# Performance work log

Measured on AMD Instinct MI355X. Metric: run time of the kernel, lower is better.

The kernel has to match this reference:

```python
import jax, jax.numpy as jnp
import numpy as np

CODE_DIMS = [32, 32, 16]   # prod = 16384 out features
FEAT_DIM = 1024
EPS = 1e-6


def setup_inputs() -> dict:
    key = jax.random.key(0)
    kx, kw = jax.random.split(key)
    x = jax.random.normal(kx, (4, 2048, FEAT_DIM), dtype=jnp.float32)
    # per-chunk trunc-normal init like _init_weights: std = sqrt(2/(feat_dim+code_dim)), clipped at +-3 std
    parts = []
    for i, cd in enumerate(CODE_DIMS):
        std = float(np.sqrt(2.0 / (FEAT_DIM + cd)))
        parts.append(std * jax.random.truncated_normal(
            jax.random.fold_in(kw, i), -3.0, 3.0, (cd, FEAT_DIM), dtype=jnp.float32))
    weight = jnp.concatenate(parts, axis=0)  # (sum(code_dims)=80, feat_dim)
    return {"x": x, "weight": weight}


def _rms_norm(y):
    var = jnp.mean(y * y, axis=-1, keepdims=True) + EPS
    return y * jax.lax.rsqrt(var)


def reference(x, weight):
    # split weight rows into the low-rank factors
    a, b, c = jnpp_split = jnp.split(weight, np.cumsum(CODE_DIMS)[:-1].tolist(), axis=0)
    # outer product over code dims, shared feature axis z -> dynamic weight (prod(code_dims), feat_dim)
    W = jnp.einsum('az,bz,cz->abcz', a, b, c).reshape(-1, weight.shape[-1])
    y = jnp.einsum('bsi,oi->bso', x, W)  # dense projection
    return _rms_norm(y)
```

## Files before the change

kernel.cpp:

```cpp
#include <hip/hip_runtime.h>
#include <hip/hip_bf16.h>

typedef unsigned short u16;
typedef __attribute__((ext_vector_type(8))) short bf16x8;
typedef __attribute__((ext_vector_type(4))) float f32x4;
typedef __attribute__((ext_vector_type(8))) unsigned short ushort8;

#define FEAT 1024
#define NOUT 16384
#define EPS 1e-6f
#define NT 16

#define GLOBAL_AS __attribute__((address_space(1)))
#define LDS_AS __attribute__((address_space(3)))

__device__ __forceinline__ void load16_to_lds(const u16* g, u16* l) {
    __builtin_amdgcn_global_load_lds((const GLOBAL_AS void*)g, (LDS_AS void*)l, 16, 0, 0);
}

__device__ __forceinline__ u16 f32_to_bf16_bits(float f) {
    __hip_bfloat16 h = __float2bfloat16(f);
    return *reinterpret_cast<u16*>(&h);
}

__device__ __forceinline__ float bf16_bits_to_f32(u16 b) {
    unsigned u = ((unsigned)b) << 16;
    float f;
    __builtin_memcpy(&f, &u, 4);
    return f;
}

__global__ void wbuild_kernel(const float* __restrict__ w, u16* __restrict__ Wb) {
    const int t  = blockIdx.x * 256 + threadIdx.x;
    const int o  = t >> 7;
    const int k0 = (t & 127) << 3;
    const int ai = o >> 9;
    const int bi = (o >> 4) & 31;
    const int ci = o & 15;
    const float* A = w + ai * FEAT + k0;
    const float* B = w + (32 + bi) * FEAT + k0;
    const float* C = w + (64 + ci) * FEAT + k0;
    ushort8 r;
#pragma unroll
    for (int j = 0; j < 8; ++j) r[j] = f32_to_bf16_bits(A[j] * B[j] * C[j]);
    *reinterpret_cast<ushort8*>(Wb + (size_t)t * 8) = r;
}

__global__ void xcast_kernel(const float* __restrict__ x, u16* __restrict__ Xb) {
    const int t = blockIdx.x * 256 + threadIdx.x;
    const float4* xv = reinterpret_cast<const float4*>(x) + (size_t)t * 2;
    const float4 f0 = xv[0];
    const float4 f1 = xv[1];
    float vals[8] = {f0.x, f0.y, f0.z, f0.w, f1.x, f1.y, f1.z, f1.w};
    ushort8 r;
#pragma unroll
    for (int j = 0; j < 8; ++j) r[j] = f32_to_bf16_bits(vals[j]);
    *reinterpret_cast<ushort8*>(Xb + (size_t)t * 8) = r;
}


#define LDSOFF(buf, isB, kh) (((buf) << 15) + ((isB) << 14) + ((kh) << 13))

#define STAGE(isB, tt, kh, buf) do {                                          \
    const u16* g = ((isB) ? gB : gA) + (size_t)(tt) * 64 + (kh) * 32 + w * 32768; \
    u16* l = lds + LDSOFF(buf, isB, kh) + w * 1024;                           \
    load16_to_lds(g, l);                                                      \
    load16_to_lds(g + 16384, l + 512);                                        \
} while (0)

#define RD_A(dst, mi, ks, buf) dst = *reinterpret_cast<const bf16x8*>(        \
    lds + LDSOFF(buf, 0, ks) + (wm * 128 + (mi) * 16 + fr) * 32 + ((kg ^ ((fr >> 1) & 3)) << 3))
#define RD_B(dst, nj, ks, buf) dst = *reinterpret_cast<const bf16x8*>(        \
    lds + LDSOFF(buf, 1, ks) + (wn * 64 + (nj) * 16 + fr) * 32 + ((kg ^ ((fr >> 1) & 3)) << 3))

#define PHASE_SYNC() do {                                                     \
    __builtin_amdgcn_sched_barrier(0);                                        \
    __builtin_amdgcn_s_barrier();                                             \
    asm volatile("s_waitcnt lgkmcnt(0)" ::: "memory");                        \
    __builtin_amdgcn_sched_barrier(0);                                        \
} while (0)

#define MFMA_Q(mibase) do {                                                   \
    __builtin_amdgcn_s_setprio(1);                                            \
    _Pragma("unroll")                                                         \
    for (int mi = 0; mi < 4; ++mi) {                                          \
        acc[(mibase)+mi][0] = __builtin_amdgcn_mfma_f32_16x16x32_bf16(a[mi], b[0], acc[(mibase)+mi][0], 0, 0, 0); \
        acc[(mibase)+mi][1] = __builtin_amdgcn_mfma_f32_16x16x32_bf16(a[mi], b[1], acc[(mibase)+mi][1], 0, 0, 0); \
        acc[(mibase)+mi][2] = __builtin_amdgcn_mfma_f32_16x16x32_bf16(a[mi], b[2], acc[(mibase)+mi][2], 0, 0, 0); \
        acc[(mibase)+mi][3] = __builtin_amdgcn_mfma_f32_16x16x32_bf16(a[mi], b[3], acc[(mibase)+mi][3], 0, 0, 0); \
    }                                                                         \
    __builtin_amdgcn_s_setprio(0);                                            \
    __builtin_amdgcn_sched_barrier(0);                                        \
    __builtin_amdgcn_s_barrier();                                             \
} while (0)

#define TILE_BODY(t, buf, nbuf) do {                                          \
                            \
    RD_A(a[0], 0, 0, buf); RD_A(a[1], 1, 0, buf);                             \
    RD_A(a[2], 2, 0, buf); RD_A(a[3], 3, 0, buf);                             \
    RD_B(b[0], 0, 0, buf); RD_B(b[1], 1, 0, buf);                             \
    RD_B(b[2], 2, 0, buf); RD_B(b[3], 3, 0, buf);                             \
    if ((t) < NT - 1) STAGE(0, (t) + 1, 1, nbuf);                             \
    PHASE_SYNC();                                                             \
    MFMA_Q(0);                                                                \
                            \
    RD_A(a[0], 4, 0, buf); RD_A(a[1], 5, 0, buf);                             \
    RD_A(a[2], 6, 0, buf); RD_A(a[3], 7, 0, buf);                             \
    if ((t) < NT - 1) STAGE(1, (t) + 1, 0, nbuf);                             \
    PHASE_SYNC();                                                             \
    MFMA_Q(4);                                                                \
                            \
    RD_A(a[0], 0, 1, buf); RD_A(a[1], 1, 1, buf);                             \
    RD_A(a[2], 2, 1, buf); RD_A(a[3], 3, 1, buf);                             \
    RD_B(b[0], 0, 1, buf); RD_B(b[1], 1, 1, buf);                             \
    RD_B(b[2], 2, 1, buf); RD_B(b[3], 3, 1, buf);                             \
    if ((t) < NT - 1) STAGE(1, (t) + 1, 1, nbuf);                             \
    PHASE_SYNC();                                                             \
    MFMA_Q(0);                                                                \
           \
    RD_A(a[0], 4, 1, buf); RD_A(a[1], 5, 1, buf);                             \
    RD_A(a[2], 6, 1, buf); RD_A(a[3], 7, 1, buf);                             \
    if ((t) < NT - 2) {                                                       \
        STAGE(0, (t) + 2, 0, buf);                                            \
        asm volatile("s_waitcnt vmcnt(2)" ::: "memory");                      \
    } else if ((t) == NT - 2) {                                               \
        asm volatile("s_waitcnt vmcnt(0)" ::: "memory");                      \
    }                                                                         \
    PHASE_SYNC();                                                             \
    MFMA_Q(4);                                                                \
} while (0)

__global__ __launch_bounds__(512, 2) void gemm_kernel(const u16* __restrict__ Xb,
                                                      const u16* __restrict__ Wb,
                                                      u16* __restrict__ Y,
                                                      float* __restrict__ Psum) {
    __shared__ u16 lds[65536];

    const int tid  = threadIdx.x;
    const int lane = tid & 63;
    const int w    = tid >> 6;
    const int wm   = w >> 2;
    const int wn   = w & 3;
    const int fr   = lane & 15;
    const int kg   = lane >> 4;

    const int bid = blockIdx.x;
    const int xcd = bid & 7;
    const int o   = bid >> 3;
    const int cb  = xcd * 8 + (o >> 7) * 4 + (o & 3);
    const int rb  = (o >> 2) & 31;
    const int brow = rb * 256;
    const int bcol = cb * 256;

    const int srow   = lane >> 2;
    const int kchunk = (lane & 3) ^ ((lane >> 3) & 3);
    const u16* gA = Xb + (size_t)(brow + srow) * FEAT + kchunk * 8;
    const u16* gB = Wb + (size_t)(bcol + srow) * FEAT + kchunk * 8;

    f32x4 acc[8][4] = {};
    bf16x8 a[4], b[4];

    STAGE(0, 0, 0, 0);
    STAGE(0, 0, 1, 0);
    STAGE(1, 0, 0, 0);
    STAGE(1, 0, 1, 0);
    STAGE(0, 1, 0, 1);
    asm volatile("s_waitcnt vmcnt(2)" ::: "memory");
    __builtin_amdgcn_s_barrier();

    for (int tt = 0; tt < NT; tt += 2) {
        TILE_BODY(tt, 0, 1);
        TILE_BODY(tt + 1, 1, 0);
    }

    float* sspart = reinterpret_cast<float*>(lds);
    const int colbase = bcol + wn * 64 + fr;
#pragma unroll
    for (int mi = 0; mi < 8; ++mi) {
#pragma unroll
        for (int r = 0; r < 4; ++r) {
            const int lrow = wm * 128 + mi * 16 + kg * 4 + r;
            u16* yrow = Y + (size_t)(brow + lrow) * 32768 + colbase;
            float s = 0.f;
#pragma unroll
            for (int nj = 0; nj < 4; ++nj) {
                const float v = acc[mi][nj][r];
                s += v * v;
                yrow[nj * 16] = f32_to_bf16_bits(v);
            }
            s += __shfl_xor(s, 1, 64);
            s += __shfl_xor(s, 2, 64);
            s += __shfl_xor(s, 4, 64);
            s += __shfl_xor(s, 8, 64);
            if (fr == 0) sspart[lrow * 4 + wn] = s;
        }
    }
    __syncthreads();
    if (tid < 256) {
        const float* sp = sspart + tid * 4;
        Psum[(size_t)(brow + tid) * 64 + cb] = sp[0] + sp[1] + sp[2] + sp[3];
    }
}

__global__ __launch_bounds__(1024) void scale_kernel(const u16* __restrict__ Y,
                                                     const float* __restrict__ Psum,
                                                     float* __restrict__ out) {
    const int row = blockIdx.x;
    const int tid = threadIdx.x;
    const ushort8* yr = reinterpret_cast<const ushort8*>(Y + (size_t)row * 32768);
    const ushort8 v0 = yr[2 * tid];
    const ushort8 v1 = yr[2 * tid + 1];

    __shared__ float scs;
    if (tid < 64) {
        float s = Psum[(size_t)row * 64 + tid];
        s += __shfl_xor(s, 1, 64);
        s += __shfl_xor(s, 2, 64);
        s += __shfl_xor(s, 4, 64);
        s += __shfl_xor(s, 8, 64);
        s += __shfl_xor(s, 16, 64);
        s += __shfl_xor(s, 32, 64);
        if (tid == 0) scs = rsqrtf(s * (1.0f / (float)NOUT) + EPS);
    }
    asm volatile("s_waitcnt vmcnt(0)" ::: "memory");
    __syncthreads();
    const float sc = scs;

    float4* orow = reinterpret_cast<float4*>(out + (size_t)row * NOUT) + tid * 4;
    float4 o0, o1, o2, o3;
    o0.x = bf16_bits_to_f32(v0[0]) * sc; o0.y = bf16_bits_to_f32(v0[1]) * sc;
    o0.z = bf16_bits_to_f32(v0[2]) * sc; o0.w = bf16_bits_to_f32(v0[3]) * sc;
    o1.x = bf16_bits_to_f32(v0[4]) * sc; o1.y = bf16_bits_to_f32(v0[5]) * sc;
    o1.z = bf16_bits_to_f32(v0[6]) * sc; o1.w = bf16_bits_to_f32(v0[7]) * sc;
    o2.x = bf16_bits_to_f32(v1[0]) * sc; o2.y = bf16_bits_to_f32(v1[1]) * sc;
    o2.z = bf16_bits_to_f32(v1[2]) * sc; o2.w = bf16_bits_to_f32(v1[3]) * sc;
    o3.x = bf16_bits_to_f32(v1[4]) * sc; o3.y = bf16_bits_to_f32(v1[5]) * sc;
    o3.z = bf16_bits_to_f32(v1[6]) * sc; o3.w = bf16_bits_to_f32(v1[7]) * sc;
    orow[0] = o0; orow[1] = o1; orow[2] = o2; orow[3] = o3;
}

extern "C" void kernel_launch(void* const* d_in, const int* in_sizes, int n_in,
                              void* d_out, int out_size, void* d_ws, size_t ws_size,
                              hipStream_t stream) {
    const float* x = (const float*)d_in[0];
    const float* w = (const float*)d_in[1];
    float* out = (float*)d_out;

    const int M = in_sizes[0] / FEAT;

    u16* Wb = (u16*)d_ws;
    u16* Xb = (u16*)((char*)d_ws + (size_t)NOUT * FEAT * 2);
    float* Psum = (float*)((char*)d_ws + (size_t)(NOUT + M) * FEAT * 2);

    u16* Y = (u16*)d_out;

    wbuild_kernel<<<(NOUT * (FEAT / 8)) / 256, 256, 0, stream>>>(w, Wb);
    xcast_kernel<<<(M * FEAT / 8) / 256, 256, 0, stream>>>(x, Xb);

    const int nblk = (M / 256) * (NOUT / 256);
    gemm_kernel<<<nblk, 512, 0, stream>>>(Xb, Wb, Y, Psum);

    scale_kernel<<<M, 1024, 0, stream>>>(Y, Psum, out);
}
```

Before: 483.3 us.

## Reschedule LDS staging to prefetch both operands deeper with relaxed vmcnt waits

Reorders the global-to-LDS staging within each K tile so both A and B k-half 0 of the tile after next are issued earlier, and the k-half 1 loads of the next tile are issued in the first half. Global-load waits move into the MFMA phase ends and become looser (vmcnt 8 or 4 instead of 2), keeping more loads in flight. The prologue preloads an extra stage. This aims to hide global memory latency better, but the wait counts and buffer-reuse ordering must match exactly or races appear.

```diff
diff --git a/kernel.cpp b/kernel.cpp
--- a/kernel.cpp
+++ b/kernel.cpp
@@ -80,7 +80,7 @@
     __builtin_amdgcn_sched_barrier(0);                                        \
 } while (0)
 
-#define MFMA_Q(mibase) do {                                                   \
+#define MFMA_Q(mibase, WAITCODE) do {                                         \
     __builtin_amdgcn_s_setprio(1);                                            \
     _Pragma("unroll")                                                         \
     for (int mi = 0; mi < 4; ++mi) {                                          \
@@ -91,43 +91,50 @@
     }                                                                         \
     __builtin_amdgcn_s_setprio(0);                                            \
     __builtin_amdgcn_sched_barrier(0);                                        \
+    WAITCODE;                                                                 \
+    __builtin_amdgcn_sched_barrier(0);                                        \
     __builtin_amdgcn_s_barrier();                                             \
 } while (0)
 
+#define NOWAIT ((void)0)
+#define WAIT_P2(t) do {                                                       \
+    if ((t) == NT - 1) { asm volatile("s_waitcnt vmcnt(0)" ::: "memory"); }   \
+    else               { asm volatile("s_waitcnt vmcnt(8)" ::: "memory"); }   \
+} while (0)
+#define WAIT_P4(t) do {                                                       \
+    if ((t) < NT - 2)       { asm volatile("s_waitcnt vmcnt(8)" ::: "memory"); } \
+    else if ((t) == NT - 2) { asm volatile("s_waitcnt vmcnt(4)" ::: "memory"); } \
+} while (0)
+
 #define TILE_BODY(t, buf, nbuf) do {                                          \
-                            \
+                   \
     RD_A(a[0], 0, 0, buf); RD_A(a[1], 1, 0, buf);                             \
     RD_A(a[2], 2, 0, buf); RD_A(a[3], 3, 0, buf);                             \
     RD_B(b[0], 0, 0, buf); RD_B(b[1], 1, 0, buf);                             \
     RD_B(b[2], 2, 0, buf); RD_B(b[3], 3, 0, buf);                             \
     if ((t) < NT - 1) STAGE(0, (t) + 1, 1, nbuf);                             \
     PHASE_SYNC();                                                             \
-    MFMA_Q(0);                                                                \
-                            \
+    MFMA_Q(0, NOWAIT);                                                        \
+                   \
     RD_A(a[0], 4, 0, buf); RD_A(a[1], 5, 0, buf);                             \
     RD_A(a[2], 6, 0, buf); RD_A(a[3], 7, 0, buf);                             \
-    if ((t) < NT - 1) STAGE(1, (t) + 1, 0, nbuf);                             \
-    PHASE_SYNC();                                                             \
-    MFMA_Q(4);                                                                \
-                            \
+    if ((t) < NT - 1) STAGE(1, (t) + 1, 1, nbuf);                             \
+    PHASE_SYNC();                                                             \
+    MFMA_Q(4, WAIT_P2(t));                                                    \
+          \
     RD_A(a[0], 0, 1, buf); RD_A(a[1], 1, 1, buf);                             \
     RD_A(a[2], 2, 1, buf); RD_A(a[3], 3, 1, buf);                             \
     RD_B(b[0], 0, 1, buf); RD_B(b[1], 1, 1, buf);                             \
     RD_B(b[2], 2, 1, buf); RD_B(b[3], 3, 1, buf);                             \
-    if ((t) < NT - 1) STAGE(1, (t) + 1, 1, nbuf);                             \
-    PHASE_SYNC();                                                             \
-    MFMA_Q(0);                                                                \
-           \
+    if ((t) < NT - 2) STAGE(0, (t) + 2, 0, buf);                              \
+    PHASE_SYNC();                                                             \
+    MFMA_Q(0, NOWAIT);                                                        \
+                    \
     RD_A(a[0], 4, 1, buf); RD_A(a[1], 5, 1, buf);                             \
     RD_A(a[2], 6, 1, buf); RD_A(a[3], 7, 1, buf);                             \
-    if ((t) < NT - 2) {                                                       \
-        STAGE(0, (t) + 2, 0, buf);                                            \
-        asm volatile("s_waitcnt vmcnt(2)" ::: "memory");                      \
-    } else if ((t) == NT - 2) {                                               \
-        asm volatile("s_waitcnt vmcnt(0)" ::: "memory");                      \
-    }                                                                         \
-    PHASE_SYNC();                                                             \
-    MFMA_Q(4);                                                                \
+    if ((t) < NT - 2) STAGE(1, (t) + 2, 0, buf);                              \
+    PHASE_SYNC();                                                             \
+    MFMA_Q(4, WAIT_P4(t));                                                    \
 } while (0)
 
 __global__ __launch_bounds__(512, 2) void gemm_kernel(const u16* __restrict__ Xb,
@@ -161,11 +168,12 @@
     bf16x8 a[4], b[4];
 
     STAGE(0, 0, 0, 0);
+    STAGE(1, 0, 0, 0);
     STAGE(0, 0, 1, 0);
-    STAGE(1, 0, 0, 0);
     STAGE(1, 0, 1, 0);
     STAGE(0, 1, 0, 1);
-    asm volatile("s_waitcnt vmcnt(2)" ::: "memory");
+    STAGE(1, 1, 0, 1);
+    asm volatile("s_waitcnt vmcnt(8)" ::: "memory");
     __builtin_amdgcn_s_barrier();
 
     for (int tt = 0; tt < NT; tt += 2) {
```

Result: no change. 481.2 us (-0.4%).
